# Kernel tuning notes

Hardware: AMD Instinct MI355X
Metric: run time of the kernel (lower is better)

## Reference

```python
import jax, jax.numpy as jnp
import numpy as np

D_MODEL = 1024
NHEAD = 16
HEAD_DIM = D_MODEL // NHEAD


def setup_inputs() -> dict:
    key = jax.random.key(0)
    k1, k2, k3 = jax.random.split(key, 3)
    x = jax.random.normal(k1, (4, 2048, D_MODEL), dtype=jnp.float32)
    # xavier_uniform init for weights, zero bias
    lim_qkv = float(np.sqrt(6.0 / (D_MODEL + 3 * D_MODEL)))
    w_qkv = jax.random.uniform(k2, (3 * D_MODEL, D_MODEL), jnp.float32, -lim_qkv, lim_qkv)
    b_qkv = jnp.zeros((3 * D_MODEL,), jnp.float32)
    lim_o = float(np.sqrt(6.0 / (D_MODEL + D_MODEL)))
    w_o = jax.random.uniform(k3, (D_MODEL, D_MODEL), jnp.float32, -lim_o, lim_o)
    b_o = jnp.zeros((D_MODEL,), jnp.float32)
    return {"x": x, "w_qkv": w_qkv, "b_qkv": b_qkv, "w_o": w_o, "b_o": b_o}


def reference(x, w_qkv, b_qkv, w_o, b_o):
    B, S, _ = x.shape
    qkv = x @ w_qkv.T + b_qkv                      # [B,S,3D]
    qkv = qkv.reshape(B, S, NHEAD, 3 * HEAD_DIM).transpose(0, 2, 1, 3)  # [B,H,S,3d]
    q, k, v = jnp.split(qkv, 3, axis=-1)           # each [B,H,S,d]
    scale = 1.0 / jnp.sqrt(jnp.asarray(HEAD_DIM, x.dtype))
    logits = jnp.einsum('bhqd,bhkd->bhqk', q, k) * scale
    attn = jax.nn.softmax(logits, axis=-1)
    vals = jnp.einsum('bhqk,bhkd->bhqd', attn, v)  # [B,H,S,d]
    vals = vals.transpose(0, 2, 1, 3).reshape(B, S, D_MODEL)
    return vals @ w_o.T + b_o
```

## Files before the change

kernel.cpp:

```cpp
#include <hip/hip_runtime.h>
#include <hip/hip_bf16.h>
#include <stdint.h>

typedef unsigned short u16;
typedef uint32_t u32;
typedef __bf16 bf16x8 __attribute__((ext_vector_type(8)));
typedef __bf16 bf16x2v __attribute__((ext_vector_type(2)));
typedef float f32x2 __attribute__((ext_vector_type(2)));
typedef float f32x4 __attribute__((ext_vector_type(4)));
typedef float f32x16 __attribute__((ext_vector_type(16)));
typedef u16 u16x4v __attribute__((ext_vector_type(4)));
typedef u32 u32x2 __attribute__((ext_vector_type(2)));

#define AS1 __attribute__((address_space(1)))
#define AS3 __attribute__((address_space(3)))

__device__ __forceinline__ void gld_lds16(const u16* g, u16* l) {
    __builtin_amdgcn_global_load_lds((const AS1 uint32_t*)g, (AS3 uint32_t*)l, 16, 0, 0);
}

__device__ __forceinline__ u16 f2bf(float f) {
    union { float f; uint32_t u; } v; v.f = f;
    uint32_t u = v.u;
    return (u16)((u + 0x7FFFu + ((u >> 16) & 1u)) >> 16);
}

__device__ __forceinline__ u32 pkbf16(float lo, float hi) {
    f32x2 e; e[0] = lo; e[1] = hi;
    union { bf16x2v b; u32 d; } u;
    u.b = __builtin_convertvector(e, bf16x2v);
    return u.d;
}

__device__ __forceinline__ u32x2 pl32swap(u32 a, u32 b) {
#if __has_builtin(__builtin_amdgcn_permlane32_swap)
    return __builtin_amdgcn_permlane32_swap(a, b, false, false);
#else
    asm volatile("v_permlane32_swap_b32 %0, %1" : "+v"(a), "+v"(b));
    u32x2 r; r[0] = a; r[1] = b; return r;
#endif
}

#define QSCALE 0.18033688011112042f

__global__ void cast_f32_bf16(const float* __restrict__ in, u16* __restrict__ out, int n4) {
    int i = blockIdx.x * blockDim.x + threadIdx.x;
    if (i < n4) {
        float4 f = ((const float4*)in)[i];
        u16x4v o;
        o.x = f2bf(f.x); o.y = f2bf(f.y); o.z = f2bf(f.z); o.w = f2bf(f.w);
        ((u16x4v*)out)[i] = o;
    }
}

template <int MODE>
__global__ __launch_bounds__(256, 2) void gemm_bt(
    const u16* __restrict__ A, const u16* __restrict__ B,
    const float* __restrict__ bias, float* __restrict__ Cf,
    u16* __restrict__ qb, u16* __restrict__ kb, u16* __restrict__ vT,
    int K, int ldc)
{
    __shared__ __align__(16) u16 As[128 * 32];
    __shared__ __align__(16) u16 Bs[128 * 32];
    const int tid = threadIdx.x;
    const int lane = tid & 63;
    const int w = tid >> 6;
    const int wm = (w >> 1) << 6;
    const int wn = (w & 1) << 6;
    const int r = lane & 15;
    const int q = lane >> 4;

    const int nwgx = gridDim.x;
    const int flat = blockIdx.y * nwgx + blockIdx.x;
    const int cpx = (nwgx * gridDim.y) >> 3;
    const int swz = (flat & 7) * cpx + (flat >> 3);
    const int m0 = (swz / nwgx) << 7;
    const int n0 = (swz % nwgx) << 7;

    const f32x4 zero4 = {0.f, 0.f, 0.f, 0.f};
    f32x4 acc[4][4];
#pragma unroll
    for (int i = 0; i < 4; ++i)
#pragma unroll
        for (int j = 0; j < 4; ++j) acc[i][j] = zero4;

    const int nk = K >> 5;
    for (int kt = 0; kt < nk; ++kt) {
        const int kk = kt << 5;
#pragma unroll
        for (int p = 0; p < 2; ++p) {
            const int idx = (p << 8) + tid;
            const int row = idx >> 2;
            const int cg = ((idx & 3) - (row >> 1)) & 3;
            gld_lds16(A + (m0 + row) * K + kk + (cg << 3), &As[idx << 3]);
            gld_lds16(B + (n0 + row) * K + kk + (cg << 3), &Bs[idx << 3]);
        }
        __syncthreads();
        bf16x8 af[4], bf[4];
#pragma unroll
        for (int i = 0; i < 4; ++i) {
            const int ra = wm + (i << 4) + r;
            af[i] = *(const bf16x8*)&As[((ra << 2) + ((q + (ra >> 1)) & 3)) << 3];
            const int rb = wn + (i << 4) + r;
            bf[i] = *(const bf16x8*)&Bs[((rb << 2) + ((q + (rb >> 1)) & 3)) << 3];
        }
#pragma unroll
        for (int i = 0; i < 4; ++i)
#pragma unroll
            for (int j = 0; j < 4; ++j)
                acc[i][j] = __builtin_amdgcn_mfma_f32_16x16x32_bf16(af[i], bf[j], acc[i][j], 0, 0, 0);
        __syncthreads();
    }

#pragma unroll
    for (int j = 0; j < 4; ++j) {
        const int col = n0 + wn + (j << 4) + r;
        const float bv = bias[col];
        if (MODE == 0) {
#pragma unroll
            for (int i = 0; i < 4; ++i)
#pragma unroll
                for (int ii = 0; ii < 4; ++ii) {
                    const int rowg = m0 + wm + (i << 4) + (q << 2) + ii;
                    Cf[rowg * ldc + col] = acc[i][j][ii] + bv;
                }
        } else {
            const int c0 = n0 + wn + (j << 4);
            const int h = c0 / 192;
            const int rem = c0 - h * 192;
            const int region = rem >> 6;
            const int colp = (h << 6) + (rem - (region << 6)) + r;
            if (region == 0) {
#pragma unroll
                for (int i = 0; i < 4; ++i)
#pragma unroll
                    for (int ii = 0; ii < 4; ++ii) {
                        const int rowg = m0 + wm + (i << 4) + (q << 2) + ii;
                        qb[rowg * 1024 + colp] = f2bf((acc[i][j][ii] + bv) * QSCALE);
                    }
            } else if (region == 1) {
#pragma unroll
                for (int i = 0; i < 4; ++i)
#pragma unroll
                    for (int ii = 0; ii < 4; ++ii) {
                        const int rowg = m0 + wm + (i << 4) + (q << 2) + ii;
                        kb[rowg * 1024 + colp] = f2bf(acc[i][j][ii] + bv);
                    }
            } else {
#pragma unroll
                for (int i = 0; i < 4; ++i) {
                    const int rowg0 = m0 + wm + (i << 4) + (q << 2);
                    u16x4v vv;
                    vv.x = f2bf(acc[i][j][0] + bv);
                    vv.y = f2bf(acc[i][j][1] + bv);
                    vv.z = f2bf(acc[i][j][2] + bv);
                    vv.w = f2bf(acc[i][j][3] + bv);
                    *(u16x4v*)&vT[(size_t)colp * 8192 + rowg0] = vv;
                }
            }
        }
    }
}

__global__ __launch_bounds__(256, 2) void attn(
    const u16* __restrict__ qb, const u16* __restrict__ kb,
    const u16* __restrict__ vT, u16* __restrict__ vals)
{
    __shared__ __align__(16) u16 S[16384];

    const int tid  = threadIdx.x;
    const int lane = tid & 63;
    const int w    = tid >> 6;
    const int c    = lane & 31;
    const int h2   = lane >> 5;
    const int head = blockIdx.x;
    const int q0   = blockIdx.y << 8;
    const int b    = blockIdx.z;
    const size_t rowbase = (size_t)b * 2048;

#pragma unroll
    for (int p = 0; p < 8; ++p) {
        const int idx = (p << 8) + tid;
        const int row = idx >> 3;
        const int cg  = ((idx & 7) - row) & 7;
        gld_lds16(qb + (rowbase + q0 + row) * 1024 + (head << 6) + (cg << 3), &S[idx << 3]);
    }
    __syncthreads();

    bf16x8 bq[4][2];
#pragma unroll
    for (int nt = 0; nt < 2; ++nt) {
        const int qr = (w << 6) + (nt << 5) + c;
#pragma unroll
        for (int dc = 0; dc < 4; ++dc)
            bq[dc][nt] = *(const bf16x8*)&S[(qr << 6) + ((((dc << 1) + h2 + qr) & 7) << 3)];
    }
    __syncthreads();

    const int srow8 = tid >> 3;
    const int scg   = ((tid & 7) - srow8) & 7;
    const u16* gK = kb + (rowbase + srow8) * 1024 + (head << 6) + (scg << 3);
    const u16* gV = vT + (size_t)((head << 6) + srow8) * 8192 + rowbase + (scg << 3);

    {
        u16* buf = S + 8192;
        gld_lds16(gK,             &buf[tid << 3]);
        gld_lds16(gK + 32 * 1024, &buf[2048 + (tid << 3)]);
        gld_lds16(gV,             &buf[4096 + (tid << 3)]);
        gld_lds16(gV + 32 * 8192, &buf[6144 + (tid << 3)]);
    }
    __syncthreads();

    int aF[4];
#pragma unroll
    for (int i = 0; i < 4; ++i)
        aF[i] = (c << 6) + ((((i << 1) + h2 + c) & 7) << 3);

    f32x16 oacc[2][2];
    f32x2 la2[2];
    f32x16 zero16;
#pragma unroll
    for (int i = 0; i < 16; ++i) {
        zero16[i] = 0.f;
        oacc[0][0][i] = 0.f; oacc[0][1][i] = 0.f;
        oacc[1][0][i] = 0.f; oacc[1][1][i] = 0.f;
    }
    la2[0][0] = 0.f; la2[0][1] = 0.f;
    la2[1][0] = 0.f; la2[1][1] = 0.f;

    const u16* gKr = gK + 65536;
    const u16* gVr = gV + 64;

    for (int kt = 0; kt < 32; ++kt) {
        const int cur = kt & 1;
        if (kt > 0) __syncthreads();
        u16* bufP = (cur == 0) ? (S + 0) : (S + 8192);
        const u16* bufC = (cur == 0) ? (S + 8192) : (S + 0);
        if (kt < 31) {
            gld_lds16(gKr,             &bufP[tid << 3]);
            gld_lds16(gKr + 32 * 1024, &bufP[2048 + (tid << 3)]);
            gld_lds16(gVr,             &bufP[4096 + (tid << 3)]);
            gld_lds16(gVr + 32 * 8192, &bufP[6144 + (tid << 3)]);
            gKr += 65536;
            gVr += 64;
        }
        const u16* Ks  = bufC;
        const u16* VTs = bufC + 4096;

#pragma unroll
        for (int mt = 0; mt < 2; ++mt) {
            __builtin_amdgcn_s_setprio(1);
            const bf16x8 ak0 = *(const bf16x8*)&Ks[aF[0] + (mt << 11)];
            f32x16 s0 = __builtin_amdgcn_mfma_f32_32x32x16_bf16(ak0, bq[0][0], zero16, 0, 0, 0);
            f32x16 s1 = __builtin_amdgcn_mfma_f32_32x32x16_bf16(ak0, bq[0][1], zero16, 0, 0, 0);
#pragma unroll
            for (int dc = 1; dc < 4; ++dc) {
                const bf16x8 ak = *(const bf16x8*)&Ks[aF[dc] + (mt << 11)];
                s0 = __builtin_amdgcn_mfma_f32_32x32x16_bf16(ak, bq[dc][0], s0, 0, 0, 0);
                s1 = __builtin_amdgcn_mfma_f32_32x32x16_bf16(ak, bq[dc][1], s1, 0, 0, 0);
            }
            __builtin_amdgcn_s_setprio(0);

            bf16x8 av[4];
#pragma unroll
            for (int ht = 0; ht < 2; ++ht)
#pragma unroll
                for (int c16 = 0; c16 < 2; ++c16)
                    av[(ht << 1) | c16] =
                        *(const bf16x8*)&VTs[aF[(mt << 1) | c16] + (ht << 11)];

#pragma unroll
            for (int nt = 0; nt < 2; ++nt) {
                const f32x16& sv = (nt == 0) ? s0 : s1;
                u32 pk[8];
#pragma unroll
                for (int p = 0; p < 8; ++p) {
                    const float e0 = __builtin_amdgcn_exp2f(sv[2 * p]);
                    const float e1 = __builtin_amdgcn_exp2f(sv[2 * p + 1]);
                    f32x2 e2; e2[0] = e0; e2[1] = e1;
                    la2[nt] += e2;
                    pk[p] = pkbf16(e0, e1);
                }
                const u32x2 r02 = pl32swap(pk[0], pk[2]);
                const u32x2 r13 = pl32swap(pk[1], pk[3]);
                const u32x2 r46 = pl32swap(pk[4], pk[6]);
                const u32x2 r57 = pl32swap(pk[5], pk[7]);
                union { u32 d[4]; bf16x8 v; } A0, A1;
                A0.d[0] = r02[0]; A0.d[1] = r13[0]; A0.d[2] = r02[1]; A0.d[3] = r13[1];
                A1.d[0] = r46[0]; A1.d[1] = r57[0]; A1.d[2] = r46[1]; A1.d[3] = r57[1];

                __builtin_amdgcn_s_setprio(1);
#pragma unroll
                for (int ht = 0; ht < 2; ++ht) {
                    oacc[ht][nt] = __builtin_amdgcn_mfma_f32_32x32x16_bf16(av[(ht << 1) | 0], A0.v, oacc[ht][nt], 0, 0, 0);
                    oacc[ht][nt] = __builtin_amdgcn_mfma_f32_32x32x16_bf16(av[(ht << 1) | 1], A1.v, oacc[ht][nt], 0, 0, 0);
                }
                __builtin_amdgcn_s_setprio(0);
            }
        }
    }

#pragma unroll
    for (int nt = 0; nt < 2; ++nt) {
        float myl = la2[nt][0] + la2[nt][1];
        myl += __shfl_xor(myl, 32, 64);
        const float inv = 1.f / myl;
        const size_t orow = rowbase + q0 + (w << 6) + (nt << 5) + c;
#pragma unroll
        for (int ht = 0; ht < 2; ++ht)
#pragma unroll
            for (int r4 = 0; r4 < 4; ++r4) {
                u16x4v vv;
                vv.x = f2bf(oacc[ht][nt][4 * r4 + 0] * inv);
                vv.y = f2bf(oacc[ht][nt][4 * r4 + 1] * inv);
                vv.z = f2bf(oacc[ht][nt][4 * r4 + 2] * inv);
                vv.w = f2bf(oacc[ht][nt][4 * r4 + 3] * inv);
                const int hd0 = (ht << 5) + (r4 << 3) + (h2 << 2);
                *(u16x4v*)&vals[orow * 1024 + (head << 6) + hd0] = vv;
            }
    }
}

extern "C" void kernel_launch(void* const* d_in, const int* in_sizes, int n_in,
                              void* d_out, int out_size, void* d_ws, size_t ws_size,
                              hipStream_t stream) {
    (void)in_sizes; (void)n_in; (void)out_size; (void)ws_size;
    const float* x     = (const float*)d_in[0];
    const float* w_qkv = (const float*)d_in[1];
    const float* b_qkv = (const float*)d_in[2];
    const float* w_o   = (const float*)d_in[3];
    const float* b_o   = (const float*)d_in[4];
    float* out = (float*)d_out;

    char* ws = (char*)d_ws;
    u16* xb    = (u16*)(ws);
    u16* wqkvb = (u16*)(ws + (size_t)(16 << 20));
    u16* wob   = (u16*)(ws + (size_t)(22 << 20));
    u16* qb    = (u16*)(ws + (size_t)(24 << 20));
    u16* kb    = (u16*)(ws + (size_t)(40 << 20));
    u16* vTb   = (u16*)(ws + (size_t)(56 << 20));
    u16* valsb = (u16*)(ws + (size_t)(72 << 20));

    cast_f32_bf16<<<8192, 256, 0, stream>>>(x, xb, 2097152);
    cast_f32_bf16<<<3072, 256, 0, stream>>>(w_qkv, wqkvb, 786432);
    cast_f32_bf16<<<1024, 256, 0, stream>>>(w_o, wob, 262144);

    gemm_bt<1><<<dim3(24, 64), 256, 0, stream>>>(xb, wqkvb, b_qkv, nullptr,
                                                 qb, kb, vTb, 1024, 3072);

    attn<<<dim3(16, 8, 4), 256, 0, stream>>>(qb, kb, vTb, valsb);

    gemm_bt<0><<<dim3(8, 64), 256, 0, stream>>>(valsb, wob, b_o, out,
                                                nullptr, nullptr, nullptr, 1024, 1024);
}
```

Before: 268.5 us.

## Restructure attention inner loop to issue both QK tiles before softmax

The attention inner loop is reordered. All K fragments for both 32-key sub-tiles are loaded up front, both QK^T score MFMA chains are issued back to back, and then exp/pack and PV MFMAs alternate. The aim is to let the exp2/pack VALU work of one sub-tile overlap with MFMA work from the other, and to hoist LDS reads ahead of their use. It raises register pressure, since four score accumulators and more fragments stay live at once, which may hurt occupancy under launch_bounds(256,2).

```diff
diff --git a/kernel.cpp b/kernel.cpp
--- a/kernel.cpp
+++ b/kernel.cpp
@@ -39,6 +39,27 @@
     asm volatile("v_permlane32_swap_b32 %0, %1" : "+v"(a), "+v"(b));
     u32x2 r; r[0] = a; r[1] = b; return r;
 #endif
+}
+
+__device__ __forceinline__ void smpack(const f32x16& sv, f32x2& la,
+                                       bf16x8& A0v, bf16x8& A1v) {
+    u32 pk[8];
+#pragma unroll
+    for (int p = 0; p < 8; ++p) {
+        const float e0 = __builtin_amdgcn_exp2f(sv[2 * p]);
+        const float e1 = __builtin_amdgcn_exp2f(sv[2 * p + 1]);
+        f32x2 e2; e2[0] = e0; e2[1] = e1;
+        la += e2;
+        pk[p] = pkbf16(e0, e1);
+    }
+    const u32x2 r02 = pl32swap(pk[0], pk[2]);
+    const u32x2 r13 = pl32swap(pk[1], pk[3]);
+    const u32x2 r46 = pl32swap(pk[4], pk[6]);
+    const u32x2 r57 = pl32swap(pk[5], pk[7]);
+    union { u32 d[4]; bf16x8 v; } A0, A1;
+    A0.d[0] = r02[0]; A0.d[1] = r13[0]; A0.d[2] = r02[1]; A0.d[3] = r13[1];
+    A1.d[0] = r46[0]; A1.d[1] = r57[0]; A1.d[2] = r46[1]; A1.d[3] = r57[1];
+    A0v = A0.v; A1v = A1.v;
 }
 
 #define QSCALE 0.18033688011112042f
@@ -247,57 +268,69 @@
         const u16* Ks  = bufC;
         const u16* VTs = bufC + 4096;
 
-#pragma unroll
-        for (int mt = 0; mt < 2; ++mt) {
-            __builtin_amdgcn_s_setprio(1);
-            const bf16x8 ak0 = *(const bf16x8*)&Ks[aF[0] + (mt << 11)];
-            f32x16 s0 = __builtin_amdgcn_mfma_f32_32x32x16_bf16(ak0, bq[0][0], zero16, 0, 0, 0);
-            f32x16 s1 = __builtin_amdgcn_mfma_f32_32x32x16_bf16(ak0, bq[0][1], zero16, 0, 0, 0);
-#pragma unroll
-            for (int dc = 1; dc < 4; ++dc) {
-                const bf16x8 ak = *(const bf16x8*)&Ks[aF[dc] + (mt << 11)];
-                s0 = __builtin_amdgcn_mfma_f32_32x32x16_bf16(ak, bq[dc][0], s0, 0, 0, 0);
-                s1 = __builtin_amdgcn_mfma_f32_32x32x16_bf16(ak, bq[dc][1], s1, 0, 0, 0);
-            }
-            __builtin_amdgcn_s_setprio(0);
-
-            bf16x8 av[4];
-#pragma unroll
-            for (int ht = 0; ht < 2; ++ht)
-#pragma unroll
-                for (int c16 = 0; c16 < 2; ++c16)
-                    av[(ht << 1) | c16] =
-                        *(const bf16x8*)&VTs[aF[(mt << 1) | c16] + (ht << 11)];
-
-#pragma unroll
-            for (int nt = 0; nt < 2; ++nt) {
-                const f32x16& sv = (nt == 0) ? s0 : s1;
-                u32 pk[8];
-#pragma unroll
-                for (int p = 0; p < 8; ++p) {
-                    const float e0 = __builtin_amdgcn_exp2f(sv[2 * p]);
-                    const float e1 = __builtin_amdgcn_exp2f(sv[2 * p + 1]);
-                    f32x2 e2; e2[0] = e0; e2[1] = e1;
-                    la2[nt] += e2;
-                    pk[p] = pkbf16(e0, e1);
-                }
-                const u32x2 r02 = pl32swap(pk[0], pk[2]);
-                const u32x2 r13 = pl32swap(pk[1], pk[3]);
-                const u32x2 r46 = pl32swap(pk[4], pk[6]);
-                const u32x2 r57 = pl32swap(pk[5], pk[7]);
-                union { u32 d[4]; bf16x8 v; } A0, A1;
-                A0.d[0] = r02[0]; A0.d[1] = r13[0]; A0.d[2] = r02[1]; A0.d[3] = r13[1];
-                A1.d[0] = r46[0]; A1.d[1] = r57[0]; A1.d[2] = r46[1]; A1.d[3] = r57[1];
-
-                __builtin_amdgcn_s_setprio(1);
-#pragma unroll
-                for (int ht = 0; ht < 2; ++ht) {
-                    oacc[ht][nt] = __builtin_amdgcn_mfma_f32_32x32x16_bf16(av[(ht << 1) | 0], A0.v, oacc[ht][nt], 0, 0, 0);
-                    oacc[ht][nt] = __builtin_amdgcn_mfma_f32_32x32x16_bf16(av[(ht << 1) | 1], A1.v, oacc[ht][nt], 0, 0, 0);
-                }
-                __builtin_amdgcn_s_setprio(0);
-            }
-        }
+        bf16x8 akA[4], akB[4], avA[4], avB[4];
+#pragma unroll
+        for (int i = 0; i < 4; ++i) {
+            akA[i] = *(const bf16x8*)&Ks[aF[i]];
+            akB[i] = *(const bf16x8*)&Ks[aF[i] + 2048];
+        }
+#pragma unroll
+        for (int ht = 0; ht < 2; ++ht)
+#pragma unroll
+            for (int c16 = 0; c16 < 2; ++c16)
+                avA[(ht << 1) | c16] = *(const bf16x8*)&VTs[aF[c16] + (ht << 11)];
+
+        __builtin_amdgcn_s_setprio(1);
+        f32x16 sA0 = __builtin_amdgcn_mfma_f32_32x32x16_bf16(akA[0], bq[0][0], zero16, 0, 0, 0);
+        f32x16 sA1 = __builtin_amdgcn_mfma_f32_32x32x16_bf16(akA[0], bq[0][1], zero16, 0, 0, 0);
+#pragma unroll
+        for (int dc = 1; dc < 4; ++dc) {
+            sA0 = __builtin_amdgcn_mfma_f32_32x32x16_bf16(akA[dc], bq[dc][0], sA0, 0, 0, 0);
+            sA1 = __builtin_amdgcn_mfma_f32_32x32x16_bf16(akA[dc], bq[dc][1], sA1, 0, 0, 0);
+        }
+        f32x16 sB0 = __builtin_amdgcn_mfma_f32_32x32x16_bf16(akB[0], bq[0][0], zero16, 0, 0, 0);
+        f32x16 sB1 = __builtin_amdgcn_mfma_f32_32x32x16_bf16(akB[0], bq[0][1], zero16, 0, 0, 0);
+#pragma unroll
+        for (int dc = 1; dc < 4; ++dc) {
+            sB0 = __builtin_amdgcn_mfma_f32_32x32x16_bf16(akB[dc], bq[dc][0], sB0, 0, 0, 0);
+            sB1 = __builtin_amdgcn_mfma_f32_32x32x16_bf16(akB[dc], bq[dc][1], sB1, 0, 0, 0);
+        }
+        __builtin_amdgcn_s_setprio(0);
+
+        bf16x8 PA0, PA1, PB0, PB1;
+        smpack(sA0, la2[0], PA0, PA1);
+        smpack(sA1, la2[1], PB0, PB1);
+
+#pragma unroll
+        for (int ht = 0; ht < 2; ++ht)
+#pragma unroll
+            for (int c16 = 0; c16 < 2; ++c16)
+                avB[(ht << 1) | c16] = *(const bf16x8*)&VTs[aF[2 + c16] + (ht << 11)];
+
+        __builtin_amdgcn_s_setprio(1);
+        oacc[0][0] = __builtin_amdgcn_mfma_f32_32x32x16_bf16(avA[0], PA0, oacc[0][0], 0, 0, 0);
+        oacc[0][0] = __builtin_amdgcn_mfma_f32_32x32x16_bf16(avA[1], PA1, oacc[0][0], 0, 0, 0);
+        oacc[1][0] = __builtin_amdgcn_mfma_f32_32x32x16_bf16(avA[2], PA0, oacc[1][0], 0, 0, 0);
+        oacc[1][0] = __builtin_amdgcn_mfma_f32_32x32x16_bf16(avA[3], PA1, oacc[1][0], 0, 0, 0);
+        oacc[0][1] = __builtin_amdgcn_mfma_f32_32x32x16_bf16(avA[0], PB0, oacc[0][1], 0, 0, 0);
+        oacc[0][1] = __builtin_amdgcn_mfma_f32_32x32x16_bf16(avA[1], PB1, oacc[0][1], 0, 0, 0);
+        oacc[1][1] = __builtin_amdgcn_mfma_f32_32x32x16_bf16(avA[2], PB0, oacc[1][1], 0, 0, 0);
+        oacc[1][1] = __builtin_amdgcn_mfma_f32_32x32x16_bf16(avA[3], PB1, oacc[1][1], 0, 0, 0);
+        __builtin_amdgcn_s_setprio(0);
+
+        smpack(sB0, la2[0], PA0, PA1);
+        smpack(sB1, la2[1], PB0, PB1);
+
+        __builtin_amdgcn_s_setprio(1);
+        oacc[0][0] = __builtin_amdgcn_mfma_f32_32x32x16_bf16(avB[0], PA0, oacc[0][0], 0, 0, 0);
+        oacc[0][0] = __builtin_amdgcn_mfma_f32_32x32x16_bf16(avB[1], PA1, oacc[0][0], 0, 0, 0);
+        oacc[1][0] = __builtin_amdgcn_mfma_f32_32x32x16_bf16(avB[2], PA0, oacc[1][0], 0, 0, 0);
+        oacc[1][0] = __builtin_amdgcn_mfma_f32_32x32x16_bf16(avB[3], PA1, oacc[1][0], 0, 0, 0);
+        oacc[0][1] = __builtin_amdgcn_mfma_f32_32x32x16_bf16(avB[0], PB0, oacc[0][1], 0, 0, 0);
+        oacc[0][1] = __builtin_amdgcn_mfma_f32_32x32x16_bf16(avB[1], PB1, oacc[0][1], 0, 0, 0);
+        oacc[1][1] = __builtin_amdgcn_mfma_f32_32x32x16_bf16(avB[2], PB0, oacc[1][1], 0, 0, 0);
+        oacc[1][1] = __builtin_amdgcn_mfma_f32_32x32x16_bf16(avB[3], PB1, oacc[1][1], 0, 0, 0);
+        __builtin_amdgcn_s_setprio(0);
     }
 
 #pragma unroll
```

Result: no change. 269.2 us (+0.3%).

## Double-buffer GEMM LDS tiles to prefetch the next K-slice during MFMA

Applied to the files above, without the earlier changes.

The bf16 GEMM kernel now uses two LDS buffers each for A and B. A prologue loads the first K-tile, and each iteration issues the global-to-LDS loads for the next tile before running the MFMAs on the current one. This is meant to hide global load latency behind compute instead of stalling on a barrier every iteration. It doubles the GEMM's LDS footprint, and the attention softmax-pack code is moved into a helper function with no change in behaviour.

```diff
diff --git a/kernel.cpp b/kernel.cpp
--- a/kernel.cpp
+++ b/kernel.cpp
@@ -41,6 +41,27 @@
 #endif
 }
 
+__device__ __forceinline__ void smpack(const f32x16& sv, f32x2& la,
+                                       bf16x8& A0v, bf16x8& A1v) {
+    u32 pk[8];
+#pragma unroll
+    for (int p = 0; p < 8; ++p) {
+        const float e0 = __builtin_amdgcn_exp2f(sv[2 * p]);
+        const float e1 = __builtin_amdgcn_exp2f(sv[2 * p + 1]);
+        f32x2 e2; e2[0] = e0; e2[1] = e1;
+        la += e2;
+        pk[p] = pkbf16(e0, e1);
+    }
+    const u32x2 r02 = pl32swap(pk[0], pk[2]);
+    const u32x2 r13 = pl32swap(pk[1], pk[3]);
+    const u32x2 r46 = pl32swap(pk[4], pk[6]);
+    const u32x2 r57 = pl32swap(pk[5], pk[7]);
+    union { u32 d[4]; bf16x8 v; } A0, A1;
+    A0.d[0] = r02[0]; A0.d[1] = r13[0]; A0.d[2] = r02[1]; A0.d[3] = r13[1];
+    A1.d[0] = r46[0]; A1.d[1] = r57[0]; A1.d[2] = r46[1]; A1.d[3] = r57[1];
+    A0v = A0.v; A1v = A1.v;
+}
+
 #define QSCALE 0.18033688011112042f
 
 __global__ void cast_f32_bf16(const float* __restrict__ in, u16* __restrict__ out, int n4) {
@@ -60,8 +81,8 @@
     u16* __restrict__ qb, u16* __restrict__ kb, u16* __restrict__ vT,
     int K, int ldc)
 {
-    __shared__ __align__(16) u16 As[128 * 32];
-    __shared__ __align__(16) u16 Bs[128 * 32];
+    __shared__ __align__(16) u16 As[2][128 * 32];
+    __shared__ __align__(16) u16 Bs[2][128 * 32];
     const int tid = threadIdx.x;
     const int lane = tid & 63;
     const int w = tid >> 6;
@@ -77,6 +98,9 @@
     const int m0 = (swz / nwgx) << 7;
     const int n0 = (swz % nwgx) << 7;
 
+    const int srow = tid >> 1;
+    (void)srow;
+
     const f32x4 zero4 = {0.f, 0.f, 0.f, 0.f};
     f32x4 acc[4][4];
 #pragma unroll
@@ -85,24 +109,37 @@
         for (int j = 0; j < 4; ++j) acc[i][j] = zero4;
 
     const int nk = K >> 5;
+
+#pragma unroll
+    for (int p = 0; p < 2; ++p) {
+        const int idx = (p << 8) + tid;
+        const int row = idx >> 2;
+        const int cg = ((idx & 3) - (row >> 1)) & 3;
+        gld_lds16(A + (m0 + row) * K + (cg << 3), &As[0][idx << 3]);
+        gld_lds16(B + (n0 + row) * K + (cg << 3), &Bs[0][idx << 3]);
+    }
+    __syncthreads();
+
     for (int kt = 0; kt < nk; ++kt) {
-        const int kk = kt << 5;
-#pragma unroll
-        for (int p = 0; p < 2; ++p) {
-            const int idx = (p << 8) + tid;
-            const int row = idx >> 2;
-            const int cg = ((idx & 3) - (row >> 1)) & 3;
-            gld_lds16(A + (m0 + row) * K + kk + (cg << 3), &As[idx << 3]);
-            gld_lds16(B + (n0 + row) * K + kk + (cg << 3), &Bs[idx << 3]);
-        }
-        __syncthreads();
+        const int cur = kt & 1;
+        if (kt + 1 < nk) {
+            const int kk = (kt + 1) << 5;
+#pragma unroll
+            for (int p = 0; p < 2; ++p) {
+                const int idx = (p << 8) + tid;
+                const int row = idx >> 2;
+                const int cg = ((idx & 3) - (row >> 1)) & 3;
+                gld_lds16(A + (m0 + row) * K + kk + (cg << 3), &As[cur ^ 1][idx << 3]);
+                gld_lds16(B + (n0 + row) * K + kk + (cg << 3), &Bs[cur ^ 1][idx << 3]);
+            }
+        }
         bf16x8 af[4], bf[4];
 #pragma unroll
         for (int i = 0; i < 4; ++i) {
             const int ra = wm + (i << 4) + r;
-            af[i] = *(const bf16x8*)&As[((ra << 2) + ((q + (ra >> 1)) & 3)) << 3];
+            af[i] = *(const bf16x8*)&As[cur][((ra << 2) + ((q + (ra >> 1)) & 3)) << 3];
             const int rb = wn + (i << 4) + r;
-            bf[i] = *(const bf16x8*)&Bs[((rb << 2) + ((q + (rb >> 1)) & 3)) << 3];
+            bf[i] = *(const bf16x8*)&Bs[cur][((rb << 2) + ((q + (rb >> 1)) & 3)) << 3];
         }
 #pragma unroll
         for (int i = 0; i < 4; ++i)
@@ -272,28 +309,14 @@
 #pragma unroll
             for (int nt = 0; nt < 2; ++nt) {
                 const f32x16& sv = (nt == 0) ? s0 : s1;
-                u32 pk[8];
-#pragma unroll
-                for (int p = 0; p < 8; ++p) {
-                    const float e0 = __builtin_amdgcn_exp2f(sv[2 * p]);
-                    const float e1 = __builtin_amdgcn_exp2f(sv[2 * p + 1]);
-                    f32x2 e2; e2[0] = e0; e2[1] = e1;
-                    la2[nt] += e2;
-                    pk[p] = pkbf16(e0, e1);
-                }
-                const u32x2 r02 = pl32swap(pk[0], pk[2]);
-                const u32x2 r13 = pl32swap(pk[1], pk[3]);
-                const u32x2 r46 = pl32swap(pk[4], pk[6]);
-                const u32x2 r57 = pl32swap(pk[5], pk[7]);
-                union { u32 d[4]; bf16x8 v; } A0, A1;
-                A0.d[0] = r02[0]; A0.d[1] = r13[0]; A0.d[2] = r02[1]; A0.d[3] = r13[1];
-                A1.d[0] = r46[0]; A1.d[1] = r57[0]; A1.d[2] = r46[1]; A1.d[3] = r57[1];
+                bf16x8 A0v, A1v;
+                smpack(sv, la2[nt], A0v, A1v);
 
                 __builtin_amdgcn_s_setprio(1);
 #pragma unroll
                 for (int ht = 0; ht < 2; ++ht) {
-                    oacc[ht][nt] = __builtin_amdgcn_mfma_f32_32x32x16_bf16(av[(ht << 1) | 0], A0.v, oacc[ht][nt], 0, 0, 0);
-                    oacc[ht][nt] = __builtin_amdgcn_mfma_f32_32x32x16_bf16(av[(ht << 1) | 1], A1.v, oacc[ht][nt], 0, 0, 0);
+                    oacc[ht][nt] = __builtin_amdgcn_mfma_f32_32x32x16_bf16(av[(ht << 1) | 0], A0v, oacc[ht][nt], 0, 0, 0);
+                    oacc[ht][nt] = __builtin_amdgcn_mfma_f32_32x32x16_bf16(av[(ht << 1) | 1], A1v, oacc[ht][nt], 0, 0, 0);
                 }
                 __builtin_amdgcn_s_setprio(0);
             }
```

Measured after the change: 276.0 us. +2.8%, slower.
